# Kernel tuning notes

Measured on AMD Instinct MI355X. Metric: run time of the kernel, lower is better.

## Reference

```python
import jax, jax.numpy as jnp
import numpy as np

EPS = 1e-12  # F.normalize eps

def _l2norm(x, axis=-1):
    n = jnp.sqrt(jnp.sum(x * x, axis=axis, keepdims=True))
    return x / jnp.maximum(n, EPS)

def setup_inputs() -> dict:
    key = jax.random.key(0)
    k1, k2 = jax.random.split(key)
    N, D, C = 262144, 128, 1024
    embeddings = jax.random.normal(k1, (N, D), dtype=jnp.float32)
    labels = jax.random.randint(k2, (N,), 0, C, dtype=jnp.int64)
    return {"embeddings": embeddings, "labels": labels, "num_classes": C}

def reference(embeddings, labels, num_classes):
    # Normalize all embeddings: [N, D]
    emb = _l2norm(embeddings, axis=1)
    # Per-class segment sums and counts (replaces python loop over unique labels)
    sums = jax.ops.segment_sum(emb, labels, num_segments=num_classes)          # [C, D]
    counts = jax.ops.segment_sum(jnp.ones((emb.shape[0],), emb.dtype), labels,
                                 num_segments=num_classes)                     # [C]
    safe_counts = jnp.maximum(counts, 1.0)
    prototypes = _l2norm(sums / safe_counts[:, None], axis=1)                  # [C, D]
    # cosine sim of each sample to its class prototype
    sim = jnp.sum(emb * prototypes[labels], axis=1)                           # [N]
    # per-class mean of (1 - sim)
    loss_sums = jax.ops.segment_sum(1.0 - sim, labels, num_segments=num_classes)
    per_class = loss_sums / safe_counts                                        # [C]
    valid = (counts >= 2.0).astype(emb.dtype)                                  # classes with >=2 samples
    n_valid = jnp.sum(valid)
    loss = jnp.sum(per_class * valid) / jnp.maximum(n_valid, 1.0)
    return jnp.where(n_valid > 0, loss, jnp.zeros((), emb.dtype))
```

## Files before the change

### kernel.cpp

```cpp
#include <hip/hip_runtime.h>
#include <math.h>

#define NUM_CLASSES 1024
#define HIST_CHUNK 2048
#define NB 128

__device__ __forceinline__ int detect_mode32(const int* __restrict__ l) {
    return (l[1] | l[3] | l[5] | l[7] | l[9] | l[11] | l[13] | l[15]) != 0;
}

__device__ __forceinline__ int get_label(const int* __restrict__ l, int i, int mode32) {
    return l[mode32 ? i : (i << 1)] & (NUM_CLASSES - 1);
}

__global__ void hist_kernel(const int* __restrict__ labels, int n,
                            int* __restrict__ pT) {
    __shared__ int h[NUM_CLASSES];
    const int mode32 = detect_mode32(labels);
    for (int i = threadIdx.x; i < NUM_CLASSES; i += blockDim.x) h[i] = 0;
    __syncthreads();
    const int base = blockIdx.x * HIST_CHUNK;
    for (int k = threadIdx.x; k < HIST_CHUNK; k += blockDim.x) {
        int i = base + k;
        if (i < n) atomicAdd(&h[get_label(labels, i, mode32)], 1);
    }
    __syncthreads();
    for (int c = threadIdx.x; c < NUM_CLASSES; c += blockDim.x)
        pT[c * NB + blockIdx.x] = h[c];
}

__global__ __launch_bounds__(512) void scanA_kernel(int* __restrict__ pT,
                                                    int* __restrict__ totals) {
    const int wave = threadIdx.x >> 6;
    const int lane = threadIdx.x & 63;
    const int c = blockIdx.x * 8 + wave;
    int* p = pT + c * NB;
    const int v0 = p[2 * lane];
    const int v1 = p[2 * lane + 1];
    int s = v0 + v1;
    #pragma unroll
    for (int d = 1; d < 64; d <<= 1) {
        int t = __shfl_up(s, d, 64);
        if (lane >= d) s += t;
    }
    const int base = s - v0 - v1;
    p[2 * lane]     = base;
    p[2 * lane + 1] = base + v0;
    if (lane == 63) totals[c] = s;
}

__global__ void scanB_kernel(const int* __restrict__ totals,
                             int* __restrict__ offsets,
                             int* __restrict__ counts,
                             float* __restrict__ accum,
                             int* __restrict__ ticket) {
    __shared__ int tmp[NUM_CLASSES];
    const int c = threadIdx.x;
    const int v = totals[c];
    tmp[c] = v;
    __syncthreads();
    for (int off = 1; off < NUM_CLASSES; off <<= 1) {
        int add = (c >= off) ? tmp[c - off] : 0;
        __syncthreads();
        tmp[c] += add;
        __syncthreads();
    }
    offsets[c] = tmp[c] - v;
    counts[c]  = v;
    if (c == 0) { accum[0] = 0.0f; accum[1] = 0.0f; *ticket = 0; }
}

__global__ void scatter_kernel(const int* __restrict__ labels, int n,
                               const int* __restrict__ pT,
                               const int* __restrict__ offsets,
                               int* __restrict__ sorted) {
    __shared__ int cur[NUM_CLASSES];
    const int mode32 = detect_mode32(labels);
    for (int c = threadIdx.x; c < NUM_CLASSES; c += blockDim.x)
        cur[c] = offsets[c] + pT[c * NB + blockIdx.x];
    __syncthreads();
    const int base = blockIdx.x * HIST_CHUNK;
    for (int k = threadIdx.x; k < HIST_CHUNK; k += blockDim.x) {
        int i = base + k;
        if (i < n) {
            int pos = atomicAdd(&cur[get_label(labels, i, mode32)], 1);
            sorted[pos] = i;
        }
    }
}

#define WPB 8
__global__ __launch_bounds__(512) void class_sum_kernel(
        const float* __restrict__ emb,
        const int* __restrict__ sorted,
        const int* __restrict__ offsets,
        const int* __restrict__ counts,
        float* __restrict__ accum,
        int* __restrict__ ticket,
        float* __restrict__ out) {
    const int c     = blockIdx.x;
    const int start = offsets[c];
    const int count = counts[c];
    const int wave  = threadIdx.x >> 6;
    const int lane  = threadIdx.x & 63;
    const int g     = lane >> 4;
    const int sub   = lane & 15;

    float4 aLo = make_float4(0.f, 0.f, 0.f, 0.f);
    float4 aHi = make_float4(0.f, 0.f, 0.f, 0.f);

    for (int r = wave * 4 + g; r < count; r += WPB * 4) {
        const int idx = sorted[start + r];
        const float4* row = (const float4*)(emb + (size_t)idx * 128);
        float4 v0 = row[sub];
        float4 v1 = row[sub + 16];
        float sq = v0.x*v0.x + v0.y*v0.y + v0.z*v0.z + v0.w*v0.w
                 + v1.x*v1.x + v1.y*v1.y + v1.z*v1.z + v1.w*v1.w;
        sq += __shfl_xor(sq, 1, 64);
        sq += __shfl_xor(sq, 2, 64);
        sq += __shfl_xor(sq, 4, 64);
        sq += __shfl_xor(sq, 8, 64);
        float inv = 1.0f / fmaxf(sqrtf(sq), 1e-12f);
        aLo.x += v0.x * inv; aLo.y += v0.y * inv; aLo.z += v0.z * inv; aLo.w += v0.w * inv;
        aHi.x += v1.x * inv; aHi.y += v1.y * inv; aHi.z += v1.z * inv; aHi.w += v1.w * inv;
    }

    __shared__ float s[WPB * 4][16][8];
    {
        float* dst = s[wave * 4 + g][sub];
        dst[0] = aLo.x; dst[1] = aLo.y; dst[2] = aLo.z; dst[3] = aLo.w;
        dst[4] = aHi.x; dst[5] = aHi.y; dst[6] = aHi.z; dst[7] = aHi.w;
    }
    __syncthreads();

    __shared__ float red[128];
    if (threadIdx.x < 128) {
        const int d  = threadIdx.x;
        const int dd = d & 63;
        const int sb = dd >> 2;
        const int j  = (d >> 6) * 4 + (dd & 3);
        float t = 0.0f;
        #pragma unroll
        for (int k = 0; k < WPB * 4; k++) t += s[k][sb][j];
        red[d] = t * t;
    }
    __syncthreads();
    if (threadIdx.x < 64) {
        float x = red[threadIdx.x] + red[threadIdx.x + 64];
        #pragma unroll
        for (int off = 32; off; off >>= 1) x += __shfl_xor(x, off, 64);
        if (threadIdx.x == 0) {
            if (count >= 2) {
                float nrm = sqrtf(x);
                float per_class = ((float)count - nrm) / (float)count;
                atomicAdd(&accum[0], per_class);
                atomicAdd(&accum[1], 1.0f);
            }
            __threadfence();
            int old = atomicAdd(ticket, 1);
            if (old == NUM_CLASSES - 1) {
                float ls = atomicAdd(&accum[0], 0.0f);
                float nv = atomicAdd(&accum[1], 0.0f);
                out[0] = (nv > 0.0f) ? (ls / nv) : 0.0f;
            }
        }
    }
}

extern "C" void kernel_launch(void* const* d_in, const int* in_sizes, int n_in,
                              void* d_out, int out_size, void* d_ws, size_t ws_size,
                              hipStream_t stream) {
    const float* emb  = (const float*)d_in[0];
    const int* labels = (const int*)d_in[1];
    const int n = in_sizes[1];

    char* ws = (char*)d_ws;
    int*   counts  = (int*)(ws + 0);
    int*   offsets = (int*)(ws + 4096);
    int*   totals  = (int*)(ws + 8192);
    float* accum   = (float*)(ws + 12288);
    int*   ticket  = (int*)(ws + 12304);
    int*   sorted  = (int*)(ws + 16384);
    int*   pT      = (int*)(ws + 16384 + (size_t)n * 4);

    hist_kernel <<<NB, 256, 0, stream>>>(labels, n, pT);
    scanA_kernel<<<NB, 512, 0, stream>>>(pT, totals);
    scanB_kernel<<<1, NUM_CLASSES, 0, stream>>>(totals, offsets, counts, accum, ticket);
    scatter_kernel<<<NB, 256, 0, stream>>>(labels, n, pT, offsets, sorted);
    class_sum_kernel<<<NUM_CLASSES, 512, 0, stream>>>(emb, sorted, offsets, counts,
                                                      accum, ticket, (float*)d_out);
}
```

Measured before the change: 253.4 us.

## Replace counting-sort gather with precomputed norms and LDS atomic class-sum accumulation

Removes the histogram/scan/scatter sorting pipeline. A first kernel computes per-row inverse norms and class counts. A second kernel accumulates normalized rows into per-class sums in shared memory with swizzled float atomics, split across dimension groups and label halves, then flushes them to global memory with atomics. A small finalize kernel computes per-class prototype norms and the mean loss using the identity that the sum of similarities equals the norm of the class sum. This trades the random gathers and multiple launches for extra streaming reads of embeddings and heavy shared-memory atomic traffic, and adds nondeterministic float summation order.

```diff
diff --git a/kernel.cpp b/kernel.cpp
--- a/kernel.cpp
+++ b/kernel.cpp
@@ -2,8 +2,7 @@
 #include <math.h>
 
 #define NUM_CLASSES 1024
-#define HIST_CHUNK 2048
-#define NB 128
+#define CHUNK 4096
 
 __device__ __forceinline__ int detect_mode32(const int* __restrict__ l) {
     return (l[1] | l[3] | l[5] | l[7] | l[9] | l[11] | l[13] | l[15]) != 0;
@@ -13,156 +12,119 @@
     return l[mode32 ? i : (i << 1)] & (NUM_CLASSES - 1);
 }
 
-__global__ void hist_kernel(const int* __restrict__ labels, int n,
-                            int* __restrict__ pT) {
-    __shared__ int h[NUM_CLASSES];
+__global__ __launch_bounds__(256) void norm_hist_kernel(
+        const float* __restrict__ emb, const int* __restrict__ labels, int n,
+        float* __restrict__ inv_norm, int* __restrict__ counts) {
+    __shared__ int hist[NUM_CLASSES];
     const int mode32 = detect_mode32(labels);
-    for (int i = threadIdx.x; i < NUM_CLASSES; i += blockDim.x) h[i] = 0;
+    for (int c = threadIdx.x; c < NUM_CLASSES; c += 256) hist[c] = 0;
     __syncthreads();
-    const int base = blockIdx.x * HIST_CHUNK;
-    for (int k = threadIdx.x; k < HIST_CHUNK; k += blockDim.x) {
-        int i = base + k;
-        if (i < n) atomicAdd(&h[get_label(labels, i, mode32)], 1);
+    const int wave = threadIdx.x >> 6;
+    const int lane = threadIdx.x & 63;
+    const int half = lane >> 5;
+    const int l32  = lane & 31;
+    const float4* emb4 = (const float4*)emb;
+    const int base = blockIdx.x * 128;
+    #pragma unroll 4
+    for (int it = 0; it < 16; ++it) {
+        int r = base + it * 8 + wave * 2 + half;
+        if (r < n) {
+            float4 v = emb4[(size_t)r * 32 + l32];
+            float sq = v.x*v.x + v.y*v.y + v.z*v.z + v.w*v.w;
+            sq += __shfl_xor(sq, 1, 64);
+            sq += __shfl_xor(sq, 2, 64);
+            sq += __shfl_xor(sq, 4, 64);
+            sq += __shfl_xor(sq, 8, 64);
+            sq += __shfl_xor(sq, 16, 64);
+            if (l32 == 0) {
+                inv_norm[r] = 1.0f / fmaxf(sqrtf(sq), 1e-12f);
+                atomicAdd(&hist[get_label(labels, r, mode32)], 1);
+            }
+        }
     }
     __syncthreads();
-    for (int c = threadIdx.x; c < NUM_CLASSES; c += blockDim.x)
-        pT[c * NB + blockIdx.x] = h[c];
-}
-
-__global__ __launch_bounds__(512) void scanA_kernel(int* __restrict__ pT,
-                                                    int* __restrict__ totals) {
-    const int wave = threadIdx.x >> 6;
-    const int lane = threadIdx.x & 63;
-    const int c = blockIdx.x * 8 + wave;
-    int* p = pT + c * NB;
-    const int v0 = p[2 * lane];
-    const int v1 = p[2 * lane + 1];
-    int s = v0 + v1;
-    #pragma unroll
-    for (int d = 1; d < 64; d <<= 1) {
-        int t = __shfl_up(s, d, 64);
-        if (lane >= d) s += t;
-    }
-    const int base = s - v0 - v1;
-    p[2 * lane]     = base;
-    p[2 * lane + 1] = base + v0;
-    if (lane == 63) totals[c] = s;
-}
-
-__global__ void scanB_kernel(const int* __restrict__ totals,
-                             int* __restrict__ offsets,
-                             int* __restrict__ counts,
-                             float* __restrict__ accum,
-                             int* __restrict__ ticket) {
-    __shared__ int tmp[NUM_CLASSES];
-    const int c = threadIdx.x;
-    const int v = totals[c];
-    tmp[c] = v;
-    __syncthreads();
-    for (int off = 1; off < NUM_CLASSES; off <<= 1) {
-        int add = (c >= off) ? tmp[c - off] : 0;
-        __syncthreads();
-        tmp[c] += add;
-        __syncthreads();
-    }
-    offsets[c] = tmp[c] - v;
-    counts[c]  = v;
-    if (c == 0) { accum[0] = 0.0f; accum[1] = 0.0f; *ticket = 0; }
-}
-
-__global__ void scatter_kernel(const int* __restrict__ labels, int n,
-                               const int* __restrict__ pT,
-                               const int* __restrict__ offsets,
-                               int* __restrict__ sorted) {
-    __shared__ int cur[NUM_CLASSES];
-    const int mode32 = detect_mode32(labels);
-    for (int c = threadIdx.x; c < NUM_CLASSES; c += blockDim.x)
-        cur[c] = offsets[c] + pT[c * NB + blockIdx.x];
-    __syncthreads();
-    const int base = blockIdx.x * HIST_CHUNK;
-    for (int k = threadIdx.x; k < HIST_CHUNK; k += blockDim.x) {
-        int i = base + k;
-        if (i < n) {
-            int pos = atomicAdd(&cur[get_label(labels, i, mode32)], 1);
-            sorted[pos] = i;
-        }
+    for (int c = threadIdx.x; c < NUM_CLASSES; c += 256) {
+        int h = hist[c];
+        if (h) atomicAdd(&counts[c], h);
     }
 }
 
-#define WPB 8
-__global__ __launch_bounds__(512) void class_sum_kernel(
-        const float* __restrict__ emb,
-        const int* __restrict__ sorted,
-        const int* __restrict__ offsets,
-        const int* __restrict__ counts,
-        float* __restrict__ accum,
-        int* __restrict__ ticket,
-        float* __restrict__ out) {
-    const int c     = blockIdx.x;
-    const int start = offsets[c];
-    const int count = counts[c];
-    const int wave  = threadIdx.x >> 6;
-    const int lane  = threadIdx.x & 63;
-    const int g     = lane >> 4;
-    const int sub   = lane & 15;
-
-    float4 aLo = make_float4(0.f, 0.f, 0.f, 0.f);
-    float4 aHi = make_float4(0.f, 0.f, 0.f, 0.f);
-
-    for (int r = wave * 4 + g; r < count; r += WPB * 4) {
-        const int idx = sorted[start + r];
-        const float4* row = (const float4*)(emb + (size_t)idx * 128);
-        float4 v0 = row[sub];
-        float4 v1 = row[sub + 16];
-        float sq = v0.x*v0.x + v0.y*v0.y + v0.z*v0.z + v0.w*v0.w
-                 + v1.x*v1.x + v1.y*v1.y + v1.z*v1.z + v1.w*v1.w;
-        sq += __shfl_xor(sq, 1, 64);
-        sq += __shfl_xor(sq, 2, 64);
-        sq += __shfl_xor(sq, 4, 64);
-        sq += __shfl_xor(sq, 8, 64);
-        float inv = 1.0f / fmaxf(sqrtf(sq), 1e-12f);
-        aLo.x += v0.x * inv; aLo.y += v0.y * inv; aLo.z += v0.z * inv; aLo.w += v0.w * inv;
-        aHi.x += v1.x * inv; aHi.y += v1.y * inv; aHi.z += v1.z * inv; aHi.w += v1.w * inv;
-    }
-
-    __shared__ float s[WPB * 4][16][8];
-    {
-        float* dst = s[wave * 4 + g][sub];
-        dst[0] = aLo.x; dst[1] = aLo.y; dst[2] = aLo.z; dst[3] = aLo.w;
-        dst[4] = aHi.x; dst[5] = aHi.y; dst[6] = aHi.z; dst[7] = aHi.w;
+__global__ __launch_bounds__(1024) void accum_kernel(
+        const float* __restrict__ emb, const int* __restrict__ labels, int n,
+        const float* __restrict__ inv_norm, float* __restrict__ sums) {
+    __shared__ float lds[512 * 32];
+    const int mode32 = detect_mode32(labels);
+    const int dg    = blockIdx.x & 3;
+    const int half  = (blockIdx.x >> 2) & 1;
+    const int chunk = blockIdx.x >> 3;
+    for (int t = threadIdx.x; t < 512 * 32; t += 1024) lds[t] = 0.0f;
+    __syncthreads();
+    const int wave = threadIdx.x >> 6;
+    const int lane = threadIdx.x & 63;
+    const int sj   = lane >> 3;
+    const int j    = lane & 7;
+    const float4* emb4 = (const float4*)emb;
+    const int base = chunk * CHUNK;
+    for (int it = 0; it < CHUNK / 128; ++it) {
+        int i = base + it * 128 + wave * 8 + sj;
+        if (i < n) {
+            int lab = get_label(labels, i, mode32);
+            if ((lab >> 9) == half) {
+                float inv = inv_norm[i];
+                float4 v = emb4[(size_t)i * 32 + dg * 8 + j];
+                int cl = lab & 511;
+                int sw = lab & 31;
+                float* row = &lds[cl << 5];
+                int o = j << 2;
+                atomicAdd(&row[(o + 0) ^ sw], v.x * inv);
+                atomicAdd(&row[(o + 1) ^ sw], v.y * inv);
+                atomicAdd(&row[(o + 2) ^ sw], v.z * inv);
+                atomicAdd(&row[(o + 3) ^ sw], v.w * inv);
+            }
+        }
     }
     __syncthreads();
+    for (int t = threadIdx.x; t < 512 * 32; t += 1024) {
+        int cl = t >> 5, p = t & 31;
+        int jd = p ^ (cl & 31);
+        unsafeAtomicAdd(&sums[(size_t)(half * 512 + cl) * 128 + dg * 32 + jd], lds[t]);
+    }
+}
 
-    __shared__ float red[128];
-    if (threadIdx.x < 128) {
-        const int d  = threadIdx.x;
-        const int dd = d & 63;
-        const int sb = dd >> 2;
-        const int j  = (d >> 6) * 4 + (dd & 3);
-        float t = 0.0f;
-        #pragma unroll
-        for (int k = 0; k < WPB * 4; k++) t += s[k][sb][j];
-        red[d] = t * t;
+__global__ __launch_bounds__(256) void finalize_kernel(
+        const float* __restrict__ sums, const int* __restrict__ counts,
+        float* __restrict__ accum, int* __restrict__ ticket,
+        float* __restrict__ out) {
+    const int wave = threadIdx.x >> 6;
+    const int lane = threadIdx.x & 63;
+    const int g    = lane >> 4;
+    const int sub  = lane & 15;
+    const int c    = blockIdx.x * 16 + wave * 4 + g;
+    const float4* s4 = (const float4*)sums;
+    float4 a = s4[(size_t)c * 32 + sub];
+    float4 b = s4[(size_t)c * 32 + 16 + sub];
+    float sq = a.x*a.x + a.y*a.y + a.z*a.z + a.w*a.w
+             + b.x*b.x + b.y*b.y + b.z*b.z + b.w*b.w;
+    sq += __shfl_xor(sq, 1, 64);
+    sq += __shfl_xor(sq, 2, 64);
+    sq += __shfl_xor(sq, 4, 64);
+    sq += __shfl_xor(sq, 8, 64);
+    if (sub == 0) {
+        int count = counts[c];
+        if (count >= 2) {
+            float per_class = ((float)count - sqrtf(sq)) / (float)count;
+            atomicAdd(&accum[0], per_class);
+            atomicAdd(&accum[1], 1.0f);
+        }
     }
     __syncthreads();
-    if (threadIdx.x < 64) {
-        float x = red[threadIdx.x] + red[threadIdx.x + 64];
-        #pragma unroll
-        for (int off = 32; off; off >>= 1) x += __shfl_xor(x, off, 64);
-        if (threadIdx.x == 0) {
-            if (count >= 2) {
-                float nrm = sqrtf(x);
-                float per_class = ((float)count - nrm) / (float)count;
-                atomicAdd(&accum[0], per_class);
-                atomicAdd(&accum[1], 1.0f);
-            }
-            __threadfence();
-            int old = atomicAdd(ticket, 1);
-            if (old == NUM_CLASSES - 1) {
-                float ls = atomicAdd(&accum[0], 0.0f);
-                float nv = atomicAdd(&accum[1], 0.0f);
-                out[0] = (nv > 0.0f) ? (ls / nv) : 0.0f;
-            }
+    if (threadIdx.x == 0) {
+        __threadfence();
+        int old = atomicAdd(ticket, 1);
+        if (old == (int)gridDim.x - 1) {
+            float ls = atomicAdd(&accum[0], 0.0f);
+            float nv = atomicAdd(&accum[1], 0.0f);
+            out[0] = (nv > 0.0f) ? (ls / nv) : 0.0f;
         }
     }
 }
@@ -175,18 +137,20 @@
     const int n = in_sizes[1];
 
     char* ws = (char*)d_ws;
-    int*   counts  = (int*)(ws + 0);
-    int*   offsets = (int*)(ws + 4096);
-    int*   totals  = (int*)(ws + 8192);
-    float* accum   = (float*)(ws + 12288);
-    int*   ticket  = (int*)(ws + 12304);
-    int*   sorted  = (int*)(ws + 16384);
-    int*   pT      = (int*)(ws + 16384 + (size_t)n * 4);
+    float* sums     = (float*)(ws);
+    int*   counts   = (int*)(ws + 524288);
+    float* accum    = (float*)(ws + 528384);
+    int*   ticket   = (int*)(ws + 528392);
+    float* inv_norm = (float*)(ws + 528640);
 
-    hist_kernel <<<NB, 256, 0, stream>>>(labels, n, pT);
-    scanA_kernel<<<NB, 512, 0, stream>>>(pT, totals);
-    scanB_kernel<<<1, NUM_CLASSES, 0, stream>>>(totals, offsets, counts, accum, ticket);
-    scatter_kernel<<<NB, 256, 0, stream>>>(labels, n, pT, offsets, sorted);
-    class_sum_kernel<<<NUM_CLASSES, 512, 0, stream>>>(emb, sorted, offsets, counts,
-                                                      accum, ticket, (float*)d_out);
+    hipMemsetAsync(ws, 0, 528640, stream);
+
+    int nb1 = (n + 127) / 128;
+    norm_hist_kernel<<<nb1, 256, 0, stream>>>(emb, labels, n, inv_norm, counts);
+
+    int chunks = (n + CHUNK - 1) / CHUNK;
+    accum_kernel<<<chunks * 8, 1024, 0, stream>>>(emb, labels, n, inv_norm, sums);
+
+    finalize_kernel<<<64, 256, 0, stream>>>(sums, counts, accum, ticket,
+                                            (float*)d_out);
 }
```

Result: slower. 414.0 us (+63.4%).

## Merge counting-sort stages into cooperative kernel and precompute row inverse norms

Applied to the files above, without the earlier changes.

Replaces the four histogram/scan/scatter kernels with one cooperative kernel that uses grid syncs. It also computes per-row inverse L2 norms with coalesced streaming reads, so the class-sum kernel no longer does per-row shuffle reductions. The class-sum loop is software-pipelined, prefetching indices and rows two stages ahead, and gets an occupancy hint. In exchange the embeddings are read twice, and the design adds grid-sync and memset costs plus global atomics on counts and cursor.

```diff
diff --git a/kernel.cpp b/kernel.cpp
--- a/kernel.cpp
+++ b/kernel.cpp
@@ -1,9 +1,12 @@
 #include <hip/hip_runtime.h>
+#include <hip/hip_cooperative_groups.h>
 #include <math.h>
 
 #define NUM_CLASSES 1024
-#define HIST_CHUNK 2048
-#define NB 128
+#define PREP_BLOCKS 512
+#define PREP_THREADS 512
+
+namespace cg = cooperative_groups;
 
 __device__ __forceinline__ int detect_mode32(const int* __restrict__ l) {
     return (l[1] | l[3] | l[5] | l[7] | l[9] | l[11] | l[13] | l[15]) != 0;
@@ -13,88 +16,130 @@
     return l[mode32 ? i : (i << 1)] & (NUM_CLASSES - 1);
 }
 
-__global__ void hist_kernel(const int* __restrict__ labels, int n,
-                            int* __restrict__ pT) {
+__device__ __forceinline__ float sumsq8(const float4 a, const float4 b) {
+    return a.x*a.x + a.y*a.y + a.z*a.z + a.w*a.w
+         + b.x*b.x + b.y*b.y + b.z*b.z + b.w*b.w;
+}
+
+__device__ __forceinline__ float red16(float sq) {
+    sq += __shfl_xor(sq, 1, 64);
+    sq += __shfl_xor(sq, 2, 64);
+    sq += __shfl_xor(sq, 4, 64);
+    sq += __shfl_xor(sq, 8, 64);
+    return sq;
+}
+
+__global__ __launch_bounds__(PREP_THREADS, 8) void prep_kernel(
+        const float* __restrict__ emb, const int* __restrict__ labels, int n,
+        int* __restrict__ counts, int* __restrict__ offsets,
+        int* __restrict__ cursor, float* __restrict__ inv_norm,
+        int* __restrict__ sorted) {
+    cg::grid_group grid = cg::this_grid();
     __shared__ int h[NUM_CLASSES];
+    __shared__ int cur[NUM_CLASSES];
+    __shared__ int tmp[PREP_THREADS];
+
     const int mode32 = detect_mode32(labels);
-    for (int i = threadIdx.x; i < NUM_CLASSES; i += blockDim.x) h[i] = 0;
-    __syncthreads();
-    const int base = blockIdx.x * HIST_CHUNK;
-    for (int k = threadIdx.x; k < HIST_CHUNK; k += blockDim.x) {
-        int i = base + k;
-        if (i < n) atomicAdd(&h[get_label(labels, i, mode32)], 1);
-    }
-    __syncthreads();
-    for (int c = threadIdx.x; c < NUM_CLASSES; c += blockDim.x)
-        pT[c * NB + blockIdx.x] = h[c];
-}
-
-__global__ __launch_bounds__(512) void scanA_kernel(int* __restrict__ pT,
-                                                    int* __restrict__ totals) {
-    const int wave = threadIdx.x >> 6;
-    const int lane = threadIdx.x & 63;
-    const int c = blockIdx.x * 8 + wave;
-    int* p = pT + c * NB;
-    const int v0 = p[2 * lane];
-    const int v1 = p[2 * lane + 1];
-    int s = v0 + v1;
-    #pragma unroll
-    for (int d = 1; d < 64; d <<= 1) {
-        int t = __shfl_up(s, d, 64);
-        if (lane >= d) s += t;
-    }
-    const int base = s - v0 - v1;
-    p[2 * lane]     = base;
-    p[2 * lane + 1] = base + v0;
-    if (lane == 63) totals[c] = s;
-}
-
-__global__ void scanB_kernel(const int* __restrict__ totals,
-                             int* __restrict__ offsets,
-                             int* __restrict__ counts,
-                             float* __restrict__ accum,
-                             int* __restrict__ ticket) {
-    __shared__ int tmp[NUM_CLASSES];
-    const int c = threadIdx.x;
-    const int v = totals[c];
-    tmp[c] = v;
-    __syncthreads();
-    for (int off = 1; off < NUM_CLASSES; off <<= 1) {
-        int add = (c >= off) ? tmp[c - off] : 0;
+    const int nb  = gridDim.x;
+    const int spb = (n + nb - 1) / nb;
+    const int s0  = blockIdx.x * spb;
+    const int s1  = min(n, s0 + spb);
+
+    for (int c = threadIdx.x; c < NUM_CLASSES; c += PREP_THREADS) h[c] = 0;
+    __syncthreads();
+    for (int i = s0 + threadIdx.x; i < s1; i += PREP_THREADS)
+        atomicAdd(&h[get_label(labels, i, mode32)], 1);
+    __syncthreads();
+    for (int c = threadIdx.x; c < NUM_CLASSES; c += PREP_THREADS) {
+        int v = h[c];
+        if (v) atomicAdd(&counts[c], v);
+    }
+
+    if (s0 < n) {
+        const int wave = threadIdx.x >> 6, lane = threadIdx.x & 63;
+        const int g = lane >> 4, sub = lane & 15;
+        const int grp = wave * 4 + g;
+        const float4* emb4 = (const float4*)emb;
+        const int nrows = s1 - s0;
+        const int quads = nrows >> 7;
+        for (int q = 0; q < quads; ++q) {
+            const int base = s0 + (q << 7) + grp;
+            const float4* p0 = emb4 + (size_t)(base     ) * 32;
+            const float4* p1 = emb4 + (size_t)(base + 32) * 32;
+            const float4* p2 = emb4 + (size_t)(base + 64) * 32;
+            const float4* p3 = emb4 + (size_t)(base + 96) * 32;
+            float4 a0 = p0[sub], a1 = p0[sub + 16];
+            float4 b0 = p1[sub], b1 = p1[sub + 16];
+            float4 c0 = p2[sub], c1 = p2[sub + 16];
+            float4 d0 = p3[sub], d1 = p3[sub + 16];
+            float sa = red16(sumsq8(a0, a1));
+            float sb = red16(sumsq8(b0, b1));
+            float sc = red16(sumsq8(c0, c1));
+            float sd = red16(sumsq8(d0, d1));
+            if (sub == 0) {
+                inv_norm[base     ] = 1.0f / fmaxf(sqrtf(sa), 1e-12f);
+                inv_norm[base + 32] = 1.0f / fmaxf(sqrtf(sb), 1e-12f);
+                inv_norm[base + 64] = 1.0f / fmaxf(sqrtf(sc), 1e-12f);
+                inv_norm[base + 96] = 1.0f / fmaxf(sqrtf(sd), 1e-12f);
+            }
+        }
+        const int done = quads << 7;
+        const int rem  = nrows - done;
+        const int kmax = (rem + 31) >> 5;
+        for (int k = 0; k < kmax; ++k) {
+            int row = s0 + done + (k << 5) + grp;
+            bool valid = row < s1;
+            int rr = valid ? row : s0;
+            const float4* p = emb4 + (size_t)rr * 32;
+            float4 a0 = p[sub], a1 = p[sub + 16];
+            float sa = red16(sumsq8(a0, a1));
+            if (valid && sub == 0)
+                inv_norm[row] = 1.0f / fmaxf(sqrtf(sa), 1e-12f);
+        }
+    }
+
+    grid.sync();
+
+    if (blockIdx.x == 0) {
+        const int t = threadIdx.x;
+        int v0 = counts[2 * t];
+        int v1 = counts[2 * t + 1];
+        int s = v0 + v1;
+        tmp[t] = s;
         __syncthreads();
-        tmp[c] += add;
-        __syncthreads();
-    }
-    offsets[c] = tmp[c] - v;
-    counts[c]  = v;
-    if (c == 0) { accum[0] = 0.0f; accum[1] = 0.0f; *ticket = 0; }
-}
-
-__global__ void scatter_kernel(const int* __restrict__ labels, int n,
-                               const int* __restrict__ pT,
-                               const int* __restrict__ offsets,
-                               int* __restrict__ sorted) {
-    __shared__ int cur[NUM_CLASSES];
-    const int mode32 = detect_mode32(labels);
-    for (int c = threadIdx.x; c < NUM_CLASSES; c += blockDim.x)
-        cur[c] = offsets[c] + pT[c * NB + blockIdx.x];
-    __syncthreads();
-    const int base = blockIdx.x * HIST_CHUNK;
-    for (int k = threadIdx.x; k < HIST_CHUNK; k += blockDim.x) {
-        int i = base + k;
-        if (i < n) {
-            int pos = atomicAdd(&cur[get_label(labels, i, mode32)], 1);
-            sorted[pos] = i;
-        }
+        for (int off = 1; off < PREP_THREADS; off <<= 1) {
+            int add = (t >= off) ? tmp[t - off] : 0;
+            __syncthreads();
+            tmp[t] += add;
+            __syncthreads();
+        }
+        int excl = tmp[t] - s;
+        offsets[2 * t]     = excl;
+        offsets[2 * t + 1] = excl + v0;
+        cursor[2 * t]      = excl;
+        cursor[2 * t + 1]  = excl + v0;
+    }
+
+    grid.sync();
+
+    for (int c = threadIdx.x; c < NUM_CLASSES; c += PREP_THREADS) {
+        int v = h[c];
+        cur[c] = v ? atomicAdd(&cursor[c], v) : 0;
+    }
+    __syncthreads();
+    for (int i = s0 + threadIdx.x; i < s1; i += PREP_THREADS) {
+        int pos = atomicAdd(&cur[get_label(labels, i, mode32)], 1);
+        sorted[pos] = i;
     }
 }
 
 #define WPB 8
-__global__ __launch_bounds__(512) void class_sum_kernel(
+__global__ __launch_bounds__(512, 4) void class_sum_kernel(
         const float* __restrict__ emb,
         const int* __restrict__ sorted,
         const int* __restrict__ offsets,
         const int* __restrict__ counts,
+        const float* __restrict__ inv_norm,
         float* __restrict__ accum,
         int* __restrict__ ticket,
         float* __restrict__ out) {
@@ -105,24 +150,54 @@
     const int lane  = threadIdx.x & 63;
     const int g     = lane >> 4;
     const int sub   = lane & 15;
+    const int r0    = wave * 4 + g;
+
+    const float4* emb4 = (const float4*)emb;
+    const int* sp = sorted + start;
 
     float4 aLo = make_float4(0.f, 0.f, 0.f, 0.f);
     float4 aHi = make_float4(0.f, 0.f, 0.f, 0.f);
-
-    for (int r = wave * 4 + g; r < count; r += WPB * 4) {
-        const int idx = sorted[start + r];
-        const float4* row = (const float4*)(emb + (size_t)idx * 128);
-        float4 v0 = row[sub];
-        float4 v1 = row[sub + 16];
-        float sq = v0.x*v0.x + v0.y*v0.y + v0.z*v0.z + v0.w*v0.w
-                 + v1.x*v1.x + v1.y*v1.y + v1.z*v1.z + v1.w*v1.w;
-        sq += __shfl_xor(sq, 1, 64);
-        sq += __shfl_xor(sq, 2, 64);
-        sq += __shfl_xor(sq, 4, 64);
-        sq += __shfl_xor(sq, 8, 64);
-        float inv = 1.0f / fmaxf(sqrtf(sq), 1e-12f);
-        aLo.x += v0.x * inv; aLo.y += v0.y * inv; aLo.z += v0.z * inv; aLo.w += v0.w * inv;
-        aHi.x += v1.x * inv; aHi.y += v1.y * inv; aHi.z += v1.z * inv; aHi.w += v1.w * inv;
+    const int FULL = count >> 5;
+
+    int iA0 = (0 < FULL) ? sp[r0]      : 0;
+    int iA1 = (1 < FULL) ? sp[r0 + 32] : 0;
+    const float4* pA0 = emb4 + (size_t)iA0 * 32;
+    const float4* pA1 = emb4 + (size_t)iA1 * 32;
+    float4 a00 = pA0[sub], a01 = pA0[sub + 16];
+    float4 a10 = pA1[sub], a11 = pA1[sub + 16];
+    float  wA0 = (0 < FULL) ? inv_norm[iA0] : 0.0f;
+    float  wA1 = (1 < FULL) ? inv_norm[iA1] : 0.0f;
+    int iB0 = (2 < FULL) ? sp[r0 + 64] : 0;
+    int iB1 = (3 < FULL) ? sp[r0 + 96] : 0;
+
+    const int STAGES = (FULL + 1) >> 1;
+    for (int s = 0; s < STAGES; ++s) {
+        const int tn = 2 * s + 2;
+        const float4* pB0 = emb4 + (size_t)iB0 * 32;
+        const float4* pB1 = emb4 + (size_t)iB1 * 32;
+        float4 b00 = pB0[sub], b01 = pB0[sub + 16];
+        float4 b10 = pB1[sub], b11 = pB1[sub + 16];
+        float  wB0 = (tn     < FULL) ? inv_norm[iB0] : 0.0f;
+        float  wB1 = (tn + 1 < FULL) ? inv_norm[iB1] : 0.0f;
+        int iC0 = (tn + 2 < FULL) ? sp[r0 + 32 * (tn + 2)] : 0;
+        int iC1 = (tn + 3 < FULL) ? sp[r0 + 32 * (tn + 3)] : 0;
+        aLo.x += a00.x * wA0; aLo.y += a00.y * wA0; aLo.z += a00.z * wA0; aLo.w += a00.w * wA0;
+        aHi.x += a01.x * wA0; aHi.y += a01.y * wA0; aHi.z += a01.z * wA0; aHi.w += a01.w * wA0;
+        aLo.x += a10.x * wA1; aLo.y += a10.y * wA1; aLo.z += a10.z * wA1; aLo.w += a10.w * wA1;
+        aHi.x += a11.x * wA1; aHi.y += a11.y * wA1; aHi.z += a11.z * wA1; aHi.w += a11.w * wA1;
+        a00 = b00; a01 = b01; a10 = b10; a11 = b11;
+        wA0 = wB0; wA1 = wB1; iB0 = iC0; iB1 = iC1;
+    }
+    {
+        const int r = r0 + 32 * FULL;
+        if (r < count) {
+            const int idx = sp[r];
+            const float4* p = emb4 + (size_t)idx * 32;
+            float4 a0 = p[sub], a1 = p[sub + 16];
+            float w = inv_norm[idx];
+            aLo.x += a0.x * w; aLo.y += a0.y * w; aLo.z += a0.z * w; aLo.w += a0.w * w;
+            aHi.x += a1.x * w; aHi.y += a1.y * w; aHi.z += a1.z * w; aHi.w += a1.w * w;
+        }
     }
 
     __shared__ float s[WPB * 4][16][8];
@@ -139,10 +214,10 @@
         const int dd = d & 63;
         const int sb = dd >> 2;
         const int j  = (d >> 6) * 4 + (dd & 3);
-        float t = 0.0f;
+        float tt = 0.0f;
         #pragma unroll
-        for (int k = 0; k < WPB * 4; k++) t += s[k][sb][j];
-        red[d] = t * t;
+        for (int k = 0; k < WPB * 4; k++) tt += s[k][sb][j];
+        red[d] = tt * tt;
     }
     __syncthreads();
     if (threadIdx.x < 64) {
@@ -172,21 +247,26 @@
                               hipStream_t stream) {
     const float* emb  = (const float*)d_in[0];
     const int* labels = (const int*)d_in[1];
-    const int n = in_sizes[1];
+    int n = in_sizes[1];
 
     char* ws = (char*)d_ws;
-    int*   counts  = (int*)(ws + 0);
-    int*   offsets = (int*)(ws + 4096);
-    int*   totals  = (int*)(ws + 8192);
-    float* accum   = (float*)(ws + 12288);
-    int*   ticket  = (int*)(ws + 12304);
-    int*   sorted  = (int*)(ws + 16384);
-    int*   pT      = (int*)(ws + 16384 + (size_t)n * 4);
-
-    hist_kernel <<<NB, 256, 0, stream>>>(labels, n, pT);
-    scanA_kernel<<<NB, 512, 0, stream>>>(pT, totals);
-    scanB_kernel<<<1, NUM_CLASSES, 0, stream>>>(totals, offsets, counts, accum, ticket);
-    scatter_kernel<<<NB, 256, 0, stream>>>(labels, n, pT, offsets, sorted);
-    class_sum_kernel<<<NUM_CLASSES, 512, 0, stream>>>(emb, sorted, offsets, counts,
-                                                      accum, ticket, (float*)d_out);
-}
+    int*   counts   = (int*)(ws + 0);
+    int*   offsets  = (int*)(ws + 4096);
+    int*   cursor   = (int*)(ws + 8192);
+    float* accum    = (float*)(ws + 12288);
+    int*   ticket   = (int*)(ws + 12296);
+    float* inv_norm = (float*)(ws + 16384);
+    int*   sorted   = (int*)(ws + 16384 + (size_t)n * 4);
+
+    hipMemsetAsync(ws, 0, 16384, stream);
+
+    void* args[] = { (void*)&emb, (void*)&labels, (void*)&n,
+                     (void*)&counts, (void*)&offsets, (void*)&cursor,
+                     (void*)&inv_norm, (void*)&sorted };
+    hipLaunchCooperativeKernel((void*)prep_kernel, dim3(PREP_BLOCKS),
+                               dim3(PREP_THREADS), args, 0, stream);
+
+    class_sum_kernel<<<NUM_CLASSES, 512, 0, stream>>>(emb, sorted, offsets,
+                                                      counts, inv_norm, accum,
+                                                      ticket, (float*)d_out);
+}
```

Result: slower. 391.5 us (+54.5%).

## Prefetch embedding rows into LDS with triple-buffered direct global-to-LDS loads

Applied to the files above, without the earlier changes.

The class-sum kernel now caches each class's sorted index list in shared memory and streams embedding rows into a per-wave triple-buffered LDS ring using global_load_lds. Explicit vmcnt and lgkmcnt waits with sched barriers keep several row loads in flight while the current batch is normalized and accumulated. Swizzled chunk mapping is meant to avoid LDS bank conflicts. It uses about 50KB of LDS per block and hand-managed waitcounts, which may limit occupancy and is fragile.

```diff
diff --git a/kernel.cpp b/kernel.cpp
--- a/kernel.cpp
+++ b/kernel.cpp
@@ -4,6 +4,7 @@
 #define NUM_CLASSES 1024
 #define HIST_CHUNK 2048
 #define NB 128
+#define WPB 8
 
 __device__ __forceinline__ int detect_mode32(const int* __restrict__ l) {
     return (l[1] | l[3] | l[5] | l[7] | l[9] | l[11] | l[13] | l[15]) != 0;
@@ -89,8 +90,36 @@
     }
 }
 
-#define WPB 8
-__global__ __launch_bounds__(512) void class_sum_kernel(
+__device__ __forceinline__ float sumsq8(const float4 a, const float4 b) {
+    return a.x*a.x + a.y*a.y + a.z*a.z + a.w*a.w
+         + b.x*b.x + b.y*b.y + b.z*b.z + b.w*b.w;
+}
+
+__device__ __forceinline__ float red16(float sq) {
+    sq += __shfl_xor(sq, 1, 64);
+    sq += __shfl_xor(sq, 2, 64);
+    sq += __shfl_xor(sq, 4, 64);
+    sq += __shfl_xor(sq, 8, 64);
+    return sq;
+}
+
+__device__ __forceinline__ void stage_batch(
+        const float* __restrict__ emb, const int* __restrict__ ids_lds,
+        const int* __restrict__ sorted_g, int cached, int start,
+        int batch, int count, int srow, int schunk, char* buf) {
+    const int rid = (batch << 2) + srow;
+    const int rc  = (rid < count) ? rid : 0;
+    const int idx = cached ? ids_lds[rc] : sorted_g[start + rc];
+    const char* gp = (const char*)(emb + (size_t)idx * 128) + (schunk << 4);
+    __builtin_amdgcn_global_load_lds(
+        (const __attribute__((address_space(1))) void*)gp,
+        (__attribute__((address_space(3))) void*)buf, 16, 0, 0);
+    __builtin_amdgcn_global_load_lds(
+        (const __attribute__((address_space(1))) void*)(gp + 256),
+        (__attribute__((address_space(3))) void*)(buf + 1024), 16, 0, 0);
+}
+
+__global__ __launch_bounds__(512, 4) void class_sum_kernel(
         const float* __restrict__ emb,
         const int* __restrict__ sorted,
         const int* __restrict__ offsets,
@@ -98,6 +127,7 @@
         float* __restrict__ accum,
         int* __restrict__ ticket,
         float* __restrict__ out) {
+    __shared__ __align__(16) char smem[51200];
     const int c     = blockIdx.x;
     const int start = offsets[c];
     const int count = counts[c];
@@ -106,43 +136,68 @@
     const int g     = lane >> 4;
     const int sub   = lane & 15;
 
+    int*  ids   = (int*)(smem + 49152);
+    char* wbase = smem + wave * 6144;
+
+    const int cached = (count <= 512);
+    const int cmax   = cached ? count : 512;
+    for (int r = threadIdx.x; r < cmax; r += 512) ids[r] = sorted[start + r];
+    __syncthreads();
+
+    const int sprime = (lane ^ (lane >> 3)) & 63;
+    const int srow   = sprime & 3;
+    const int schunk = sprime >> 2;
+    const int sidx = (sub << 2) | g;
+    const int t1   = sidx ^ (sidx >> 3);
+
     float4 aLo = make_float4(0.f, 0.f, 0.f, 0.f);
     float4 aHi = make_float4(0.f, 0.f, 0.f, 0.f);
 
-    for (int r = wave * 4 + g; r < count; r += WPB * 4) {
-        const int idx = sorted[start + r];
-        const float4* row = (const float4*)(emb + (size_t)idx * 128);
-        float4 v0 = row[sub];
-        float4 v1 = row[sub + 16];
-        float sq = v0.x*v0.x + v0.y*v0.y + v0.z*v0.z + v0.w*v0.w
-                 + v1.x*v1.x + v1.y*v1.y + v1.z*v1.z + v1.w*v1.w;
-        sq += __shfl_xor(sq, 1, 64);
-        sq += __shfl_xor(sq, 2, 64);
-        sq += __shfl_xor(sq, 4, 64);
-        sq += __shfl_xor(sq, 8, 64);
-        float inv = 1.0f / fmaxf(sqrtf(sq), 1e-12f);
-        aLo.x += v0.x * inv; aLo.y += v0.y * inv; aLo.z += v0.z * inv; aLo.w += v0.w * inv;
-        aHi.x += v1.x * inv; aHi.y += v1.y * inv; aHi.z += v1.z * inv; aHi.w += v1.w * inv;
-    }
-
-    __shared__ float s[WPB * 4][16][8];
+    if (count > 0) {
+        const int nb = (count + 3) >> 2;
+        const int Kw = (nb > wave) ? ((nb - 1 - wave) / WPB + 1) : 0;
+        stage_batch(emb, ids, sorted, cached, start, wave,           count, srow, schunk, wbase);
+        stage_batch(emb, ids, sorted, cached, start, wave + WPB,     count, srow, schunk, wbase + 2048);
+        stage_batch(emb, ids, sorted, cached, start, wave + 2 * WPB, count, srow, schunk, wbase + 4096);
+        for (int k = 0; k < Kw; ++k) {
+            asm volatile("s_waitcnt vmcnt(4)" ::: "memory");
+            __builtin_amdgcn_sched_barrier(0);
+            const float4* buf = (const float4*)(wbase + (k % 3) * 2048);
+            float4 a0 = buf[t1];
+            float4 a1 = buf[64 + t1];
+            asm volatile("s_waitcnt lgkmcnt(0)" ::: "memory");
+            __builtin_amdgcn_sched_barrier(0);
+            stage_batch(emb, ids, sorted, cached, start,
+                        wave + (k + 3) * WPB, count, srow, schunk,
+                        wbase + (k % 3) * 2048);
+            const int rid = ((wave + k * WPB) << 2) + g;
+            float sq  = red16(sumsq8(a0, a1));
+            float inv = ((rid < count) ? 1.0f : 0.0f) / fmaxf(sqrtf(sq), 1e-12f);
+            aLo.x += a0.x * inv; aLo.y += a0.y * inv; aLo.z += a0.z * inv; aLo.w += a0.w * inv;
+            aHi.x += a1.x * inv; aHi.y += a1.y * inv; aHi.z += a1.z * inv; aHi.w += a1.w * inv;
+        }
+    }
+    asm volatile("s_waitcnt vmcnt(0)" ::: "memory");
+    __syncthreads();
+
+    float (*sred)[16][8] = (float (*)[16][8])smem;
     {
-        float* dst = s[wave * 4 + g][sub];
+        float* dst = sred[wave * 4 + g][sub];
         dst[0] = aLo.x; dst[1] = aLo.y; dst[2] = aLo.z; dst[3] = aLo.w;
         dst[4] = aHi.x; dst[5] = aHi.y; dst[6] = aHi.z; dst[7] = aHi.w;
     }
     __syncthreads();
 
-    __shared__ float red[128];
+    float* red = (float*)(smem + 16384);
     if (threadIdx.x < 128) {
         const int d  = threadIdx.x;
         const int dd = d & 63;
         const int sb = dd >> 2;
         const int j  = (d >> 6) * 4 + (dd & 3);
-        float t = 0.0f;
+        float tt = 0.0f;
         #pragma unroll
-        for (int k = 0; k < WPB * 4; k++) t += s[k][sb][j];
-        red[d] = t * t;
+        for (int k = 0; k < WPB * 4; k++) tt += sred[k][sb][j];
+        red[d] = tt * tt;
     }
     __syncthreads();
     if (threadIdx.x < 64) {
```

After: 248.6 us. No clear change (-1.9%).
